# Kernel tuning notes

Measured on AMD Instinct MI355X. Metric: run time of the kernel, lower is better.

The kernel has to match this reference:

```python
import jax, jax.numpy as jnp
import numpy as np

INTERVAL = 4
UPSCALE = 4
K = 3              # sample_size
SAMPLERS = 3
Q = 2 ** INTERVAL                 # 16
L = 2 ** (8 - INTERVAL) + 1       # 17
PAD = K - 1
B, H, W = 4, 512, 512

_STRIDES = np.array([L ** 3, L ** 2, L, 1], dtype=np.int32)


def ste_round(x):
    # straight-through round (round_func in the torch code)
    return x + jax.lax.stop_gradient(jnp.round(x) - x)


def fix_weight(w):
    return jnp.clip(ste_round(w * 127.0), -127.0, 127.0)


def sample(img, sw, sb):
    # unfold(K, K-1) + conv-per-patch + fold is exactly a VALID conv.
    # img: (B,1,h+PAD,w+PAD); sw: (4,1,K,K) -> a,b,c,d each (B,1,h,w)
    out = jax.lax.conv_general_dilated(img, sw, (1, 1), 'VALID',
        dimension_numbers=('NCHW', 'OIHW', 'NCHW')) + sb[None, :, None, None]
    return out[:, 0:1], out[:, 1:2], out[:, 2:3], out[:, 3:4]


def interp(lut, res_w, sw, sb, scale, img_in, prev_img):
    # InterpTorchBatch: 4D simplex interpolation into the quantized LUT.
    # Sorted-simplex form is equivalent to the 24-case masked torch code
    # (ties yield zero-weight terms, so tie ordering is irrelevant).
    w = fix_weight(lut)                                       # (L^4, scale*scale)
    a, b, c, d = sample(img_in, sw, sb)
    if prev_img is not None:
        rw = jnp.clip(res_w, 0.0, 1.0)
        pa, pb, pc, pd = sample(prev_img, sw, sb)
        a = rw[0, 0] * pa + (1.0 - rw[0, 0]) * a
        b = rw[0, 1] * pb + (1.0 - rw[0, 1]) * b
        c = rw[1, 0] * pc + (1.0 - rw[1, 0]) * c
        d = rw[1, 1] * pd + (1.0 - rw[1, 1]) * d
    vals = jnp.concatenate([a, b, c, d], axis=1).transpose(0, 2, 3, 1)   # (B,h,w,4)
    lo = jnp.floor_divide(vals, float(Q)).astype(jnp.int32)
    f = jnp.mod(vals, float(Q))
    order = jnp.argsort(-f, axis=-1)                          # fractional parts, descending
    fs = jnp.take_along_axis(f, order, axis=-1)
    strides = jnp.asarray(_STRIDES)
    base = jnp.sum(lo * strides, axis=-1)                     # flat index of p0000
    inc = jnp.cumsum(strides[order], axis=-1)
    verts = jnp.concatenate([base[..., None], base[..., None] + inc], axis=-1)  # (B,h,w,5)
    ws = jnp.concatenate([float(Q) - fs[..., :1], fs[..., :-1] - fs[..., 1:], fs[..., -1:]], axis=-1)
    p = w[verts]                                              # gather: (B,h,w,5,scale*scale)
    out = jnp.einsum('bhwv,bhwvk->bhwk', ws, p) / float(Q)
    bb, hh, ww, _ = out.shape
    out = out.reshape(bb, hh, ww, scale, scale).transpose(0, 1, 3, 2, 4)
    return out.reshape(bb, 1, hh * scale, ww * scale)


def _pad_rot(x, r):
    return jnp.pad(jnp.rot90(x, r, axes=(2, 3)),
                   ((0, 0), (0, 0), (0, PAD), (0, PAD)), mode='edge')


def rotate_input(lut, scale, sw, sb, x, res_w, prev_x):
    pred = jnp.zeros((), jnp.float32)
    for r in range(4):
        pr = None if prev_x is None else _pad_rot(prev_x, r)
        pred = pred + jnp.rot90(
            interp(lut, res_w, sw, sb, scale, _pad_rot(x, r), pr),
            (4 - r) % 4, axes=(2, 3))
        pred = ste_round(pred)
    return pred


def autolut_forward(x, lut0, lut1, samp0, samp1, sbias0, sbias1, resw1):
    x = x * 255.0
    # stage 0: scale 1, no residual, bias 127
    pred = 0.0
    for s in range(SAMPLERS):
        pred = pred + rotate_input(lut0[s], 1, samp0[s], sbias0[s], x, None, None)
    prev_x = x
    x = ste_round(jnp.clip(pred / (SAMPLERS * 4.0) + 127.0, 0.0, 255.0))
    # stage 1 (last): upscale, residual blend with previous stage input
    pred = 0.0
    for s in range(SAMPLERS):
        pred = pred + rotate_input(lut1[s], UPSCALE, samp1[s], sbias1[s], x, resw1[s], prev_x)
    x = ste_round(jnp.clip(pred / float(SAMPLERS), 0.0, 255.0))
    return x / 255.0   # phase == 'train'


def setup_inputs() -> dict:
    key = jax.random.key(0)
    ks = jax.random.split(key, 6)
    x = jax.random.uniform(ks[0], (B, 1, H, W), dtype=jnp.float32)
    lut0 = jax.random.uniform(ks[1], (SAMPLERS, L ** 4, 1), jnp.float32, -1.0, 1.0)
    lut1 = jax.random.uniform(ks[2], (SAMPLERS, L ** 4, UPSCALE * UPSCALE), jnp.float32, -1.0, 1.0)

    def mk_sampler(k):
        w = jax.random.normal(k, (SAMPLERS, 4, 1, K, K), dtype=jnp.float32)
        # convex combination of patch pixels -> sampled values stay in [0,255]
        return jax.nn.softmax(w.reshape(SAMPLERS, 4, -1), axis=-1).reshape(SAMPLERS, 4, 1, K, K)

    samp0 = mk_sampler(ks[3])
    samp1 = mk_sampler(ks[4])
    sbias0 = jnp.zeros((SAMPLERS, 4), jnp.float32)
    sbias1 = jnp.zeros((SAMPLERS, 4), jnp.float32)
    resw1 = jax.random.uniform(ks[5], (SAMPLERS, 2, 2), dtype=jnp.float32)
    return {"x": x, "lut0": lut0, "lut1": lut1, "samp0": samp0, "samp1": samp1,
            "sbias0": sbias0, "sbias1": sbias1, "resw1": resw1}


def reference(x, lut0, lut1, samp0, samp1, sbias0, sbias1, resw1):
    return autolut_forward(x, lut0, lut1, samp0, samp1, sbias0, sbias1, resw1)
```

## Files before the change

### kernel.cpp

```cpp
#include <hip/hip_runtime.h>
#include <math.h>

static constexpr int B_ = 4;
static constexpr int N_ = 512;
static constexpr int N4_ = 2048;
static constexpr int NPIX = B_ * N_ * N_;
static constexpr int LUT_ROWS = 83521;
static constexpr int SPAD = 83584;
static constexpr int ST0 = 4913, ST1 = 289, ST2 = 17, ST3 = 1;

__device__ __forceinline__ float fixw(float v) {
    v = rintf(v * 127.0f);
    return fminf(fmaxf(v, -127.0f), 127.0f);
}

__global__ void fix_lut0_kernel(const float* __restrict__ in, char* __restrict__ out) {
    int t = blockIdx.x * blockDim.x + threadIdx.x;
    int s = blockIdx.y;
    if (t < LUT_ROWS) out[(size_t)s * SPAD + t] = (char)(int)fixw(in[(size_t)s * LUT_ROWS + t]);
}

__global__ void fix_lut1_kernel(const float4* __restrict__ in, uchar4* __restrict__ out, int n4) {
    int t = blockIdx.x * blockDim.x + threadIdx.x;
    if (t < n4) {
        float4 v = in[t];
        uchar4 o;
        o.x = (unsigned char)((int)fixw(v.x) + 127);
        o.y = (unsigned char)((int)fixw(v.y) + 127);
        o.z = (unsigned char)((int)fixw(v.z) + 127);
        o.w = (unsigned char)((int)fixw(v.w) + 127);
        out[t] = o;
    }
}

struct Simplex {
    int v[5];
    float w[5];
};

__device__ __forceinline__ Simplex simplex4(float a, float b, float c, float d) {
    float fl0 = floorf(a * 0.0625f), fl1 = floorf(b * 0.0625f),
          fl2 = floorf(c * 0.0625f), fl3 = floorf(d * 0.0625f);
    float f[4] = { a - 16.0f * fl0, b - 16.0f * fl1, c - 16.0f * fl2, d - 16.0f * fl3 };
    int l0 = min(max((int)fl0, 0), 15);
    int l1 = min(max((int)fl1, 0), 15);
    int l2 = min(max((int)fl2, 0), 15);
    int l3 = min(max((int)fl3, 0), 15);
    int st[4] = { ST0, ST1, ST2, ST3 };
#define CSW(A, Bq) { if (f[A] < f[Bq]) { float tf = f[A]; f[A] = f[Bq]; f[Bq] = tf; \
                                         int ts = st[A]; st[A] = st[Bq]; st[Bq] = ts; } }
    CSW(0, 1) CSW(1, 2) CSW(2, 3) CSW(0, 1) CSW(1, 2) CSW(0, 1)
#undef CSW
    Simplex s;
    s.v[0] = l0 * ST0 + l1 * ST1 + l2 * ST2 + l3;
    s.v[1] = s.v[0] + st[0];
    s.v[2] = s.v[1] + st[1];
    s.v[3] = s.v[2] + st[2];
    s.v[4] = s.v[3] + st[3];
    s.w[0] = (16.0f - f[0]) * 0.0625f;
    s.w[1] = (f[0] - f[1]) * 0.0625f;
    s.w[2] = (f[1] - f[2]) * 0.0625f;
    s.w[3] = (f[2] - f[3]) * 0.0625f;
    s.w[4] = f[3] * 0.0625f;
    return s;
}

__device__ __forceinline__ bool tap_for_r(int r, int a, int c, int& di, int& dj) {
    if (r == 0) { di = a - 2; dj = c - 2; return (a >= 2) && (c >= 2); }
    if (r == 1) { di = 2 - c; dj = a - 2; return (a >= 2) && (c <= 2); }
    if (r == 2) { di = 2 - a; dj = 2 - c; return (a <= 2) && (c <= 2); }
    di = c - 2; dj = 2 - a; return (a <= 2) && (c >= 2);
}

__device__ __forceinline__ void acc4u(unsigned int q, float wv, float* oc) {
    oc[0] = fmaf(wv, (float)(q & 0xffu), oc[0]);
    oc[1] = fmaf(wv, (float)((q >> 8) & 0xffu), oc[1]);
    oc[2] = fmaf(wv, (float)((q >> 16) & 0xffu), oc[2]);
    oc[3] = fmaf(wv, (float)(q >> 24), oc[3]);
}

__global__ __launch_bounds__(1024, 4) void stage0_kernel(
    const float* __restrict__ x,
    const char* __restrict__ lut0q,
    const float* __restrict__ samp0,
    const float* __restrict__ sbias0,
    float* __restrict__ x1)
{
    __shared__ char luts[SPAD];

    int b    = blockIdx.x >> 8;
    int tile = blockIdx.x & 255;
    int i = ((tile >> 4) << 5) + (threadIdx.x >> 5);
    int j = ((tile & 15) << 5) + (threadIdx.x & 31);
    const float* xb = x + (size_t)b * N_ * N_;

    float pred = 0.0f;
    for (int s = 0; s < 3; ++s) {
        __syncthreads();
        {
            const int4* src = (const int4*)(lut0q + (size_t)s * SPAD);
            int4* dst = (int4*)luts;
            for (int u = threadIdx.x; u < SPAD / 16; u += 1024) dst[u] = src[u];
        }
        __syncthreads();

        const float* w  = samp0 + s * 36;
        const float* sb = sbias0 + s * 4;

        float vals[4][4];
        #pragma unroll
        for (int r = 0; r < 4; ++r)
            #pragma unroll
            for (int ch = 0; ch < 4; ++ch) vals[r][ch] = 0.0f;
        #pragma unroll
        for (int a = 0; a < 5; ++a) {
            int ri = min(max(i - 2 + a, 0), N_ - 1);
            #pragma unroll
            for (int c = 0; c < 5; ++c) {
                int ci = min(max(j - 2 + c, 0), N_ - 1);
                float px = xb[ri * N_ + ci] * 255.0f;
                #pragma unroll
                for (int r = 0; r < 4; ++r) {
                    int di, dj;
                    if (tap_for_r(r, a, c, di, dj)) {
                        #pragma unroll
                        for (int ch = 0; ch < 4; ++ch)
                            vals[r][ch] += w[ch * 9 + di * 3 + dj] * px;
                    }
                }
            }
        }

        float acc = 0.0f;
        #pragma unroll
        for (int r = 0; r < 4; ++r) {
            Simplex sx = simplex4(vals[r][0] + sb[0], vals[r][1] + sb[1],
                                  vals[r][2] + sb[2], vals[r][3] + sb[3]);
            float p0 = (float)luts[sx.v[0]];
            float p1 = (float)luts[sx.v[1]];
            float p2 = (float)luts[sx.v[2]];
            float p3 = (float)luts[sx.v[3]];
            float p4 = (float)luts[sx.v[4]];
            float o = sx.w[0] * p0 + sx.w[1] * p1 + sx.w[2] * p2
                    + sx.w[3] * p3 + sx.w[4] * p4;
            acc = rintf(acc + o);
        }
        pred += acc;
    }
    x1[(size_t)b * N_ * N_ + i * N_ + j] =
        rintf(fminf(fmaxf(pred / 12.0f + 127.0f, 0.0f), 255.0f));
}

__global__ __launch_bounds__(256) void stage1_kernel(
    const float* __restrict__ x,
    const float* __restrict__ x1,
    const unsigned char* __restrict__ lut1q,
    const float* __restrict__ samp1,
    const float* __restrict__ sbias1,
    const float* __restrict__ resw1,
    float* __restrict__ out)
{
    int b    = blockIdx.x >> 10;
    int tile = blockIdx.x & 1023;
    int i = ((tile >> 5) << 4) + (threadIdx.x >> 4);
    int j = ((tile & 31) << 4) + (threadIdx.x & 15);
    const float* xb  = x  + (size_t)b * N_ * N_;
    const float* x1b = x1 + (size_t)b * N_ * N_;

    float tot[16];
    #pragma unroll
    for (int k = 0; k < 16; ++k) tot[k] = 0.0f;

    for (int s = 0; s < 3; ++s) {
        const float* w  = samp1 + s * 36;
        const float* sb = sbias1 + s * 4;
        const unsigned char* lut = lut1q + (size_t)s * LUT_ROWS * 16;
        float rw[4];
        #pragma unroll
        for (int ch = 0; ch < 4; ++ch)
            rw[ch] = fminf(fmaxf(resw1[s * 4 + ch], 0.0f), 1.0f);

        float vals[4][4];
        {
            float vc[4][4], vp[4][4];
            #pragma unroll
            for (int r = 0; r < 4; ++r)
                #pragma unroll
                for (int ch = 0; ch < 4; ++ch) { vc[r][ch] = 0.0f; vp[r][ch] = 0.0f; }
            #pragma unroll
            for (int a = 0; a < 5; ++a) {
                int ri = min(max(i - 2 + a, 0), N_ - 1);
                #pragma unroll
                for (int c = 0; c < 5; ++c) {
                    int ci = min(max(j - 2 + c, 0), N_ - 1);
                    float pc = x1b[ri * N_ + ci];
                    float pp = xb[ri * N_ + ci] * 255.0f;
                    #pragma unroll
                    for (int r = 0; r < 4; ++r) {
                        int di, dj;
                        if (tap_for_r(r, a, c, di, dj)) {
                            #pragma unroll
                            for (int ch = 0; ch < 4; ++ch) {
                                float wt = w[ch * 9 + di * 3 + dj];
                                vc[r][ch] += wt * pc;
                                vp[r][ch] += wt * pp;
                            }
                        }
                    }
                }
            }
            #pragma unroll
            for (int r = 0; r < 4; ++r)
                #pragma unroll
                for (int ch = 0; ch < 4; ++ch)
                    vals[r][ch] = rw[ch] * (vp[r][ch] + sb[ch])
                                + (1.0f - rw[ch]) * (vc[r][ch] + sb[ch]);
        }

        float acc[16];
        #pragma unroll
        for (int k = 0; k < 16; ++k) acc[k] = 0.0f;

        #pragma unroll
        for (int r = 0; r < 4; ++r) {
            Simplex sx = simplex4(vals[r][0], vals[r][1], vals[r][2], vals[r][3]);
            float oc[16];
            #pragma unroll
            for (int k = 0; k < 16; ++k) oc[k] = 0.0f;
            #pragma unroll
            for (int v = 0; v < 5; ++v) {
                const uint4 q = *(const uint4*)(lut + (size_t)sx.v[v] * 16);
                float wv = sx.w[v];
                acc4u(q.x, wv, oc);
                acc4u(q.y, wv, oc + 4);
                acc4u(q.z, wv, oc + 8);
                acc4u(q.w, wv, oc + 12);
            }
            float S = sx.w[0] + sx.w[1] + sx.w[2] + sx.w[3] + sx.w[4];
            float bias = 127.0f * S;
            #pragma unroll
            for (int k = 0; k < 16; ++k) oc[k] -= bias;
            #pragma unroll
            for (int u = 0; u < 4; ++u)
                #pragma unroll
                for (int v2 = 0; v2 < 4; ++v2) {
                    int k = 4 * u + v2;
                    int c = (r == 0) ? (4 * u + v2)
                          : (r == 1) ? (4 * (3 - v2) + u)
                          : (r == 2) ? (4 * (3 - u) + (3 - v2))
                                     : (4 * v2 + (3 - u));
                    acc[k] = rintf(acc[k] + oc[c]);
                }
        }
        #pragma unroll
        for (int k = 0; k < 16; ++k) tot[k] += acc[k];
    }

    float* ob = out + (size_t)b * N4_ * N4_ + (size_t)(i * 4) * N4_ + (j * 4);
    #pragma unroll
    for (int u = 0; u < 4; ++u) {
        float4 val;
        val.x = rintf(fminf(fmaxf(tot[4 * u + 0] / 3.0f, 0.0f), 255.0f)) * (1.0f / 255.0f);
        val.y = rintf(fminf(fmaxf(tot[4 * u + 1] / 3.0f, 0.0f), 255.0f)) * (1.0f / 255.0f);
        val.z = rintf(fminf(fmaxf(tot[4 * u + 2] / 3.0f, 0.0f), 255.0f)) * (1.0f / 255.0f);
        val.w = rintf(fminf(fmaxf(tot[4 * u + 3] / 3.0f, 0.0f), 255.0f)) * (1.0f / 255.0f);
        *(float4*)(ob + (size_t)u * N4_) = val;
    }
}

extern "C" void kernel_launch(void* const* d_in, const int* in_sizes, int n_in,
                              void* d_out, int out_size, void* d_ws, size_t ws_size,
                              hipStream_t stream) {
    const float* x      = (const float*)d_in[0];
    const float* lut0   = (const float*)d_in[1];
    const float* lut1   = (const float*)d_in[2];
    const float* samp0  = (const float*)d_in[3];
    const float* samp1  = (const float*)d_in[4];
    const float* sbias0 = (const float*)d_in[5];
    const float* sbias1 = (const float*)d_in[6];
    const float* resw1  = (const float*)d_in[7];
    float* out = (float*)d_out;
    char* ws   = (char*)d_ws;

    const int N_L1 = 3 * LUT_ROWS * 16;
    size_t off_x1 = 0;
    size_t off_l0 = (size_t)NPIX * sizeof(float);
    size_t off_l1 = (off_l0 + (size_t)3 * SPAD + 15) & ~(size_t)15;

    float* x1 = (float*)(ws + off_x1);
    char* l0q = ws + off_l0;
    unsigned char* l1q = (unsigned char*)(ws + off_l1);

    const int threads = 256;

    dim3 g0((LUT_ROWS + threads - 1) / threads, 3);
    fix_lut0_kernel<<<g0, threads, 0, stream>>>(lut0, l0q);
    fix_lut1_kernel<<<(N_L1 / 4 + threads - 1) / threads, threads, 0, stream>>>(
        (const float4*)lut1, (uchar4*)l1q, N_L1 / 4);
    stage0_kernel<<<NPIX / 1024, 1024, 0, stream>>>(x, l0q, samp0, sbias0, x1);
    stage1_kernel<<<NPIX / threads, threads, 0, stream>>>(x, x1, l1q, samp1, sbias1, resw1, out);
}
```

Before: 296.5 us.

## Hoist sampler convolutions out of sampler loops and sort simplex keys via packed doubles

Both stages now compute the 5x5 neighbourhood convolution for all three samplers in one pass, so each pixel is loaded once instead of three times. Stage 1 folds the residual blend into the input as pc + rw*(pp-pc) before the convolution, halving the multiply-adds. The simplex sort packs each fraction with its stride into a double and uses a five-comparator min/max network instead of six branchy swaps. Keeping 48 accumulators live raises register pressure, and the double-based sort relies on fractions being non-negative for the ordering to hold.

```diff
diff --git a/kernel.cpp b/kernel.cpp
--- a/kernel.cpp
+++ b/kernel.cpp
@@ -38,30 +38,45 @@
     float w[5];
 };
 
+__device__ __forceinline__ double pack_key(float f, unsigned stride) {
+    unsigned long long u = ((unsigned long long)__float_as_uint(f) << 32) | stride;
+    return __longlong_as_double((long long)u);
+}
+__device__ __forceinline__ float key_f(double k) {
+    return __uint_as_float((unsigned)((unsigned long long)__double_as_longlong(k) >> 32));
+}
+__device__ __forceinline__ int key_s(double k) {
+    return (int)(unsigned)__double_as_longlong(k);
+}
+
 __device__ __forceinline__ Simplex simplex4(float a, float b, float c, float d) {
     float fl0 = floorf(a * 0.0625f), fl1 = floorf(b * 0.0625f),
           fl2 = floorf(c * 0.0625f), fl3 = floorf(d * 0.0625f);
-    float f[4] = { a - 16.0f * fl0, b - 16.0f * fl1, c - 16.0f * fl2, d - 16.0f * fl3 };
+    float f0 = a - 16.0f * fl0, f1 = b - 16.0f * fl1,
+          f2 = c - 16.0f * fl2, f3 = d - 16.0f * fl3;
     int l0 = min(max((int)fl0, 0), 15);
     int l1 = min(max((int)fl1, 0), 15);
     int l2 = min(max((int)fl2, 0), 15);
     int l3 = min(max((int)fl3, 0), 15);
-    int st[4] = { ST0, ST1, ST2, ST3 };
-#define CSW(A, Bq) { if (f[A] < f[Bq]) { float tf = f[A]; f[A] = f[Bq]; f[Bq] = tf; \
-                                         int ts = st[A]; st[A] = st[Bq]; st[Bq] = ts; } }
-    CSW(0, 1) CSW(1, 2) CSW(2, 3) CSW(0, 1) CSW(1, 2) CSW(0, 1)
-#undef CSW
+    double k0 = pack_key(f0, (unsigned)ST0);
+    double k1 = pack_key(f1, (unsigned)ST1);
+    double k2 = pack_key(f2, (unsigned)ST2);
+    double k3 = pack_key(f3, (unsigned)ST3);
+#define CSWD(X, Y) { double mx_ = fmax(X, Y); Y = fmin(X, Y); X = mx_; }
+    CSWD(k0, k1) CSWD(k2, k3) CSWD(k0, k2) CSWD(k1, k3) CSWD(k1, k2)
+#undef CSWD
     Simplex s;
     s.v[0] = l0 * ST0 + l1 * ST1 + l2 * ST2 + l3;
-    s.v[1] = s.v[0] + st[0];
-    s.v[2] = s.v[1] + st[1];
-    s.v[3] = s.v[2] + st[2];
-    s.v[4] = s.v[3] + st[3];
-    s.w[0] = (16.0f - f[0]) * 0.0625f;
-    s.w[1] = (f[0] - f[1]) * 0.0625f;
-    s.w[2] = (f[1] - f[2]) * 0.0625f;
-    s.w[3] = (f[2] - f[3]) * 0.0625f;
-    s.w[4] = f[3] * 0.0625f;
+    s.v[1] = s.v[0] + key_s(k0);
+    s.v[2] = s.v[1] + key_s(k1);
+    s.v[3] = s.v[2] + key_s(k2);
+    s.v[4] = s.v[3] + key_s(k3);
+    float g0 = key_f(k0), g1 = key_f(k1), g2 = key_f(k2), g3 = key_f(k3);
+    s.w[0] = (16.0f - g0) * 0.0625f;
+    s.w[1] = (g0 - g1) * 0.0625f;
+    s.w[2] = (g1 - g2) * 0.0625f;
+    s.w[3] = (g2 - g3) * 0.0625f;
+    s.w[4] = g3 * 0.0625f;
     return s;
 }
 
@@ -94,7 +109,37 @@
     int j = ((tile & 15) << 5) + (threadIdx.x & 31);
     const float* xb = x + (size_t)b * N_ * N_;
 
+    float vals[3][4][4];
+    #pragma unroll
+    for (int s = 0; s < 3; ++s)
+        #pragma unroll
+        for (int r = 0; r < 4; ++r)
+            #pragma unroll
+            for (int ch = 0; ch < 4; ++ch) vals[s][r][ch] = 0.0f;
+    #pragma unroll
+    for (int a = 0; a < 5; ++a) {
+        int ri = min(max(i - 2 + a, 0), N_ - 1);
+        const float* row = xb + ri * N_;
+        #pragma unroll
+        for (int c = 0; c < 5; ++c) {
+            int ci = min(max(j - 2 + c, 0), N_ - 1);
+            float px = row[ci] * 255.0f;
+            #pragma unroll
+            for (int r = 0; r < 4; ++r) {
+                int di, dj;
+                if (tap_for_r(r, a, c, di, dj)) {
+                    #pragma unroll
+                    for (int s = 0; s < 3; ++s)
+                        #pragma unroll
+                        for (int ch = 0; ch < 4; ++ch)
+                            vals[s][r][ch] += samp0[s * 36 + ch * 9 + di * 3 + dj] * px;
+                }
+            }
+        }
+    }
+
     float pred = 0.0f;
+    #pragma unroll
     for (int s = 0; s < 3; ++s) {
         __syncthreads();
         {
@@ -104,38 +149,12 @@
         }
         __syncthreads();
 
-        const float* w  = samp0 + s * 36;
         const float* sb = sbias0 + s * 4;
-
-        float vals[4][4];
-        #pragma unroll
-        for (int r = 0; r < 4; ++r)
-            #pragma unroll
-            for (int ch = 0; ch < 4; ++ch) vals[r][ch] = 0.0f;
-        #pragma unroll
-        for (int a = 0; a < 5; ++a) {
-            int ri = min(max(i - 2 + a, 0), N_ - 1);
-            #pragma unroll
-            for (int c = 0; c < 5; ++c) {
-                int ci = min(max(j - 2 + c, 0), N_ - 1);
-                float px = xb[ri * N_ + ci] * 255.0f;
-                #pragma unroll
-                for (int r = 0; r < 4; ++r) {
-                    int di, dj;
-                    if (tap_for_r(r, a, c, di, dj)) {
-                        #pragma unroll
-                        for (int ch = 0; ch < 4; ++ch)
-                            vals[r][ch] += w[ch * 9 + di * 3 + dj] * px;
-                    }
-                }
-            }
-        }
-
         float acc = 0.0f;
         #pragma unroll
         for (int r = 0; r < 4; ++r) {
-            Simplex sx = simplex4(vals[r][0] + sb[0], vals[r][1] + sb[1],
-                                  vals[r][2] + sb[2], vals[r][3] + sb[3]);
+            Simplex sx = simplex4(vals[s][r][0] + sb[0], vals[s][r][1] + sb[1],
+                                  vals[s][r][2] + sb[2], vals[s][r][3] + sb[3]);
             float p0 = (float)luts[sx.v[0]];
             float p1 = (float)luts[sx.v[1]];
             float p2 = (float)luts[sx.v[2]];
@@ -167,55 +186,59 @@
     const float* xb  = x  + (size_t)b * N_ * N_;
     const float* x1b = x1 + (size_t)b * N_ * N_;
 
-    float tot[16];
-    #pragma unroll
-    for (int k = 0; k < 16; ++k) tot[k] = 0.0f;
-
-    for (int s = 0; s < 3; ++s) {
-        const float* w  = samp1 + s * 36;
-        const float* sb = sbias1 + s * 4;
-        const unsigned char* lut = lut1q + (size_t)s * LUT_ROWS * 16;
-        float rw[4];
+    float rw[3][4];
+    #pragma unroll
+    for (int s = 0; s < 3; ++s)
         #pragma unroll
         for (int ch = 0; ch < 4; ++ch)
-            rw[ch] = fminf(fmaxf(resw1[s * 4 + ch], 0.0f), 1.0f);
-
-        float vals[4][4];
-        {
-            float vc[4][4], vp[4][4];
-            #pragma unroll
-            for (int r = 0; r < 4; ++r)
+            rw[s][ch] = fminf(fmaxf(resw1[s * 4 + ch], 0.0f), 1.0f);
+
+    float vals[3][4][4];
+    #pragma unroll
+    for (int s = 0; s < 3; ++s)
+        #pragma unroll
+        for (int r = 0; r < 4; ++r)
+            #pragma unroll
+            for (int ch = 0; ch < 4; ++ch) vals[s][r][ch] = sbias1[s * 4 + ch];
+
+    #pragma unroll
+    for (int a = 0; a < 5; ++a) {
+        int ri = min(max(i - 2 + a, 0), N_ - 1);
+        const float* r1 = x1b + ri * N_;
+        const float* r0 = xb + ri * N_;
+        #pragma unroll
+        for (int c = 0; c < 5; ++c) {
+            int ci = min(max(j - 2 + c, 0), N_ - 1);
+            float pc = r1[ci];
+            float pp = r0[ci] * 255.0f;
+            float dq = pp - pc;
+            float q[3][4];
+            #pragma unroll
+            for (int s = 0; s < 3; ++s)
                 #pragma unroll
-                for (int ch = 0; ch < 4; ++ch) { vc[r][ch] = 0.0f; vp[r][ch] = 0.0f; }
-            #pragma unroll
-            for (int a = 0; a < 5; ++a) {
-                int ri = min(max(i - 2 + a, 0), N_ - 1);
-                #pragma unroll
-                for (int c = 0; c < 5; ++c) {
-                    int ci = min(max(j - 2 + c, 0), N_ - 1);
-                    float pc = x1b[ri * N_ + ci];
-                    float pp = xb[ri * N_ + ci] * 255.0f;
+                for (int ch = 0; ch < 4; ++ch)
+                    q[s][ch] = fmaf(rw[s][ch], dq, pc);
+            #pragma unroll
+            for (int r = 0; r < 4; ++r) {
+                int di, dj;
+                if (tap_for_r(r, a, c, di, dj)) {
                     #pragma unroll
-                    for (int r = 0; r < 4; ++r) {
-                        int di, dj;
-                        if (tap_for_r(r, a, c, di, dj)) {
-                            #pragma unroll
-                            for (int ch = 0; ch < 4; ++ch) {
-                                float wt = w[ch * 9 + di * 3 + dj];
-                                vc[r][ch] += wt * pc;
-                                vp[r][ch] += wt * pp;
-                            }
-                        }
-                    }
+                    for (int s = 0; s < 3; ++s)
+                        #pragma unroll
+                        for (int ch = 0; ch < 4; ++ch)
+                            vals[s][r][ch] += samp1[s * 36 + ch * 9 + di * 3 + dj] * q[s][ch];
                 }
             }
-            #pragma unroll
-            for (int r = 0; r < 4; ++r)
-                #pragma unroll
-                for (int ch = 0; ch < 4; ++ch)
-                    vals[r][ch] = rw[ch] * (vp[r][ch] + sb[ch])
-                                + (1.0f - rw[ch]) * (vc[r][ch] + sb[ch]);
-        }
+        }
+    }
+
+    float tot[16];
+    #pragma unroll
+    for (int k = 0; k < 16; ++k) tot[k] = 0.0f;
+
+    #pragma unroll
+    for (int s = 0; s < 3; ++s) {
+        const unsigned char* lut = lut1q + (size_t)s * LUT_ROWS * 16;
 
         float acc[16];
         #pragma unroll
@@ -223,7 +246,7 @@
 
         #pragma unroll
         for (int r = 0; r < 4; ++r) {
-            Simplex sx = simplex4(vals[r][0], vals[r][1], vals[r][2], vals[r][3]);
+            Simplex sx = simplex4(vals[s][r][0], vals[s][r][1], vals[s][r][2], vals[s][r][3]);
             float oc[16];
             #pragma unroll
             for (int k = 0; k < 16; ++k) oc[k] = 0.0f;
```

Result: no change. 294.0 us (-0.9%).
